# Kernel optimization log

Hardware: AMD Instinct MI355X
Metric: run time of the kernel (lower is better)

The kernel has to match this reference:

```python
import jax, jax.numpy as jnp
import numpy as np

EPS = 1e-5


def _mlp_bn(x, W1, b1, g, beta, W2, b2):
    # Linear -> BatchNorm1d (training: batch stats, biased var) -> ReLU -> Linear
    h = x @ W1 + b1
    mu = h.mean(axis=0)
    var = ((h - mu) ** 2).mean(axis=0)
    h = (h - mu) * jax.lax.rsqrt(var + EPS) * g + beta
    h = jax.nn.relu(h)
    return h @ W2 + b2


def setup_inputs() -> dict:
    key = jax.random.key(0)
    ks = jax.random.split(key, 16)
    B, N, D, K = 32768, 262144, 256, 100
    f32 = jnp.float32
    rn = lambda k, s, sc=1.0: jax.random.normal(k, s, f32) * sc
    inp = {
        "z1": rn(ks[0], (B, D)),
        "z2": rn(ks[1], (B, D)),
        "zn": rn(ks[2], (N, D)),
        "emb": rn(ks[3], (K, D)),
        "proj_W1": rn(ks[4], (D, D), 0.05), "proj_b1": jnp.zeros((D,), f32),
        "proj_g": jnp.ones((D,), f32), "proj_beta": jnp.zeros((D,), f32),
        "proj_W2": rn(ks[5], (D, D), 0.05), "proj_b2": jnp.zeros((D,), f32),
        "invp_W1": rn(ks[6], (D, D), 0.05), "invp_b1": jnp.zeros((D,), f32),
        "invp_g": jnp.ones((D,), f32), "invp_beta": jnp.zeros((D,), f32),
        "invp_W2": rn(ks[7], (D, D), 0.05), "invp_b2": jnp.zeros((D,), f32),
        "latt_W": rn(ks[8], (D, 6), 0.05), "latt_b": jnp.zeros((6,), f32),
        "atom_W": rn(ks[9], (D, K), 0.05), "atom_b": jnp.zeros((K,), f32),
        "scaler_mean": rn(ks[10], (6,)),
        "scaler_std": jax.random.uniform(ks[11], (6,), f32) + 0.5,
        "lscaled_lattice": rn(ks[12], (B, 6)),
        "num_atoms": jnp.full((B,), 8, jnp.int32),
        "batch_idx": (jnp.arange(N) // 8).astype(jnp.int32),
        "atomic_nums": jax.random.randint(ks[13], (N,), 0, K).astype(jnp.int32),
    }
    return inp


def reference(z1, z2, zn, emb,
              proj_W1, proj_b1, proj_g, proj_beta, proj_W2, proj_b2,
              invp_W1, invp_b1, invp_g, invp_beta, invp_W2, invp_b2,
              latt_W, latt_b, atom_W, atom_b,
              scaler_mean, scaler_std, lscaled_lattice,
              num_atoms, batch_idx, atomic_nums):
    sg = jax.lax.stop_gradient
    B = z2.shape[0]
    N = zn.shape[0]

    # ---- VQ: pairwise distances + argmin + gather (get_code_indicies/quantize) ----
    d = (jnp.sum(z2 ** 2, axis=1, keepdims=True)
         + jnp.sum(emb ** 2, axis=1)
         - 2.0 * z2 @ emb.T)                      # [B, K]
    idx = jnp.argmin(d, axis=1)                   # [B]
    quant = emb[idx]                              # [B, D]
    q_latent = jnp.mean((quant - sg(z2)) ** 2)
    e_latent = jnp.mean((z2 - sg(quant)) ** 2)
    vq_loss = q_latent + e_latent
    z2q = z2 + sg(quant - z2)                     # straight-through

    # ---- cycle losses (proj/invp MLPs with train-mode BatchNorm) ----
    p1 = _mlp_bn(z1, proj_W1, proj_b1, proj_g, proj_beta, proj_W2, proj_b2)
    loss_p = jnp.mean((p1 - z2q) ** 2)
    loss_i = jnp.mean((z1 - _mlp_bn(z2q, invp_W1, invp_b1, invp_g, invp_beta, invp_W2, invp_b2)) ** 2)
    loss_c = jnp.mean((_mlp_bn(p1, invp_W1, invp_b1, invp_g, invp_beta, invp_W2, invp_b2) - z1) ** 2)
    cycle_loss = loss_p + loss_i + loss_c

    # ---- lattice loss ----
    pred_la = z2q @ latt_W + latt_b               # [B, 6]
    target_la = (lscaled_lattice - scaler_mean) / scaler_std
    latt_loss = jnp.mean((pred_la - target_la) ** 2) * 10.0

    # ---- per-atom composition cross-entropy, graph-mean then mean ----
    logits = zn @ atom_W + atom_b                 # [N, K]
    logp = jax.nn.log_softmax(logits, axis=-1)
    ce = -jnp.take_along_axis(logp, atomic_nums[:, None].astype(jnp.int32), axis=1)[:, 0]
    sums = jax.ops.segment_sum(ce, batch_idx, num_segments=B)
    counts = jax.ops.segment_sum(jnp.ones_like(ce), batch_idx, num_segments=B)
    atom_loss = jnp.mean(sums / jnp.maximum(counts, 1.0))

    loss = cycle_loss + atom_loss + latt_loss + vq_loss
    return (loss, cycle_loss, atom_loss, latt_loss, vq_loss)
```

## Files before the change

### kernel.cpp

```cpp
#include <hip/hip_runtime.h>
#include <math.h>

#define BATCH 32768
#define DD 256
#define KC 100
#define NATOMS 262144

typedef unsigned short u16;
typedef __attribute__((ext_vector_type(8))) short bf16x8;
typedef __attribute__((ext_vector_type(4))) float f32x4;

union Pack8 { uint4 v; u16 us[8]; };

__device__ inline u16 f2b(float f) {
    unsigned u = __float_as_uint(f);
    unsigned r = (u + 0x7fffu + ((u >> 16) & 1u)) >> 16;
    return (u16)r;
}
__device__ inline float b2f(u16 x) { return __uint_as_float(((unsigned)x) << 16); }


template<int NT>
__device__ inline void block_reduce_add(float v, float* target) {
    __shared__ float red[NT];
    red[threadIdx.x] = v;
    __syncthreads();
    for (int s = NT/2; s > 0; s >>= 1) {
        if ((int)threadIdx.x < s) red[threadIdx.x] += red[threadIdx.x + s];
        __syncthreads();
    }
    if (threadIdx.x == 0) atomicAdd(target, red[0]);
}

__global__ __launch_bounds__(256) void transpose_cvt256_k(const float* __restrict__ W,
                                                          u16* __restrict__ Wt) {
    int o = blockIdx.x * 256 + threadIdx.x;
    int n = o >> 8, k = o & 255;
    Wt[o] = f2b(W[k * 256 + n]);
}
__global__ __launch_bounds__(256) void transpose_cvt_atom_k(const float* __restrict__ W,
                                                            u16* __restrict__ Wt) {
    int o = blockIdx.x * 256 + threadIdx.x;
    int n = o >> 8, k = o & 255;
    Wt[o] = (n < KC) ? f2b(W[k * KC + n]) : (u16)0;
}
__global__ __launch_bounds__(256) void embT_k(const float* __restrict__ emb,
                                              u16* __restrict__ hi, u16* __restrict__ lo) {
    int o = blockIdx.x * 256 + threadIdx.x;
    int n = o >> 8, d = o & 255;
    float v = (n < KC) ? emb[n * DD + d] : 0.f;
    u16 h = f2b(v);
    hi[o] = h;
    lo[o] = f2b(v - b2f(h));
}
__global__ __launch_bounds__(256) void cvt_bf16_k(const float* __restrict__ x,
                                                  u16* __restrict__ y, int n8) {
    int i = blockIdx.x * 256 + threadIdx.x;
    if (i < n8) {
        const float4* p = (const float4*)(x + (size_t)i * 8);
        float4 f0 = p[0], f1 = p[1];
        Pack8 pk;
        pk.us[0]=f2b(f0.x); pk.us[1]=f2b(f0.y); pk.us[2]=f2b(f0.z); pk.us[3]=f2b(f0.w);
        pk.us[4]=f2b(f1.x); pk.us[5]=f2b(f1.y); pk.us[6]=f2b(f1.z); pk.us[7]=f2b(f1.w);
        *(uint4*)(y + (size_t)i * 8) = pk.v;
    }
}
__global__ __launch_bounds__(64) void enorm_k(const float* __restrict__ emb,
                                              float* __restrict__ enorm) {
    int k = blockIdx.x, lane = threadIdx.x;
    float4 v = *(const float4*)(emb + (size_t)k * DD + lane * 4);
    float s = v.x*v.x + v.y*v.y + v.z*v.z + v.w*v.w;
    #pragma unroll
    for (int off = 1; off < 64; off <<= 1) s += __shfl_xor(s, off);
    if (lane == 0) enorm[k] = 0.5f * s;
}

__global__ __launch_bounds__(256) void vq_k(
    const float* __restrict__ z2, const u16* __restrict__ Eh, const u16* __restrict__ El,
    const float* __restrict__ enorm, int* __restrict__ idx, float* acc)
{
    __shared__ u16 Ah[64*32], Al[64*32], Bh[112*32], Bl[112*32];
    const int t = threadIdx.x;
    const int n0 = blockIdx.x * 64;
    const int lane = t & 63, wave = t >> 6;
    const int l15 = lane & 15, lg = lane >> 4;
    const int am = t >> 2, akc = t & 3;

    f32x4 dot[7];
    #pragma unroll
    for (int j = 0; j < 7; ++j) dot[j] = (f32x4){0.f, 0.f, 0.f, 0.f};

    for (int k0 = 0; k0 < DD; k0 += 32) {
        {
            const float* src = z2 + (size_t)(n0 + am) * DD + k0 + akc * 8;
            float4 f0 = *(const float4*)src;
            float4 f1 = *(const float4*)(src + 4);
            float fv[8] = {f0.x, f0.y, f0.z, f0.w, f1.x, f1.y, f1.z, f1.w};
            Pack8 ph, pl;
            #pragma unroll
            for (int e = 0; e < 8; ++e) {
                u16 h = f2b(fv[e]);
                ph.us[e] = h;
                pl.us[e] = f2b(fv[e] - b2f(h));
            }
            int off = (am * 32 + akc * 8) ^ ((am & 7) << 3);
            *(uint4*)(Ah + off) = ph.v;
            *(uint4*)(Al + off) = pl.v;
        }
        {
            int bn = t >> 2, bkc = t & 3;
            int off = (bn * 32 + bkc * 8) ^ ((bn & 7) << 3);
            *(uint4*)(Bh + off) = *(const uint4*)(Eh + bn * DD + k0 + bkc * 8);
            *(uint4*)(Bl + off) = *(const uint4*)(El + bn * DD + k0 + bkc * 8);
            int c2 = t + 256;
            if (c2 < 448) {
                int bn2 = c2 >> 2, bkc2 = c2 & 3;
                int off2 = (bn2 * 32 + bkc2 * 8) ^ ((bn2 & 7) << 3);
                *(uint4*)(Bh + off2) = *(const uint4*)(Eh + bn2 * DD + k0 + bkc2 * 8);
                *(uint4*)(Bl + off2) = *(const uint4*)(El + bn2 * DD + k0 + bkc2 * 8);
            }
        }
        __syncthreads();

        int m = wave * 16 + l15;
        int aoff = (m * 32 + lg * 8) ^ ((m & 7) << 3);
        bf16x8 ah = *(const bf16x8*)(Ah + aoff);
        bf16x8 al = *(const bf16x8*)(Al + aoff);
        #pragma unroll
        for (int j = 0; j < 7; ++j) {
            int n = j * 16 + l15;
            int boff = (n * 32 + lg * 8) ^ ((n & 7) << 3);
            bf16x8 bh = *(const bf16x8*)(Bh + boff);
            bf16x8 bl = *(const bf16x8*)(Bl + boff);
            dot[j] = __builtin_amdgcn_mfma_f32_16x16x32_bf16(ah, bh, dot[j], 0, 0, 0);
            dot[j] = __builtin_amdgcn_mfma_f32_16x16x32_bf16(ah, bl, dot[j], 0, 0, 0);
            dot[j] = __builtin_amdgcn_mfma_f32_16x16x32_bf16(al, bh, dot[j], 0, 0, 0);
        }
        __syncthreads();
    }

    float vq_local = 0.f;
    #pragma unroll
    for (int r = 0; r < 4; ++r) {
        int row = n0 + wave * 16 + lg * 4 + r;
        float bv = 3.4e38f; int bc = 1000;
        #pragma unroll
        for (int j = 0; j < 7; ++j) {
            int c = j * 16 + l15;
            if (c < KC) {
                float y = enorm[c] - dot[j][r];
                if (y < bv) { bv = y; bc = c; }
            }
        }
        #pragma unroll
        for (int off = 1; off < 16; off <<= 1) {
            float ov = __shfl_xor(bv, off);
            int   oc = __shfl_xor(bc, off);
            if (ov < bv || (ov == bv && oc < bc)) { bv = ov; bc = oc; }
        }
        float zs = 0.f;
        const float* zr = z2 + (size_t)row * DD + l15 * 16;
        #pragma unroll
        for (int u = 0; u < 4; ++u) {
            float4 v = *(const float4*)(zr + u * 4);
            zs = fmaf(v.x, v.x, fmaf(v.y, v.y, fmaf(v.z, v.z, fmaf(v.w, v.w, zs))));
        }
        #pragma unroll
        for (int off = 1; off < 16; off <<= 1) zs += __shfl_xor(zs, off);
        if (l15 == 0) {
            idx[row] = bc;
            vq_local += 2.f * bv + zs;
        }
    }
    block_reduce_add<256>(vq_local, acc + 0);
}

template<int MODE_A, int MODE_T, int WRITE_C, int DO_STATS, int DO_LOSS>
__global__ __launch_bounds__(512) void mlp_gemm(
    const void* __restrict__ Asrc, const u16* __restrict__ Wt,
    const float* __restrict__ bias,
    const float* __restrict__ cs_in, const float* __restrict__ cs2_in,
    const float* __restrict__ g_in, const float* __restrict__ beta_in,
    const int* __restrict__ gidx, const float* __restrict__ embf,
    u16* __restrict__ Cb,
    float* __restrict__ colsum, float* __restrict__ colsum2,
    const float* __restrict__ Tf, float* __restrict__ loss_acc)
{
    __shared__ u16 As[64 * 32];
    __shared__ u16 Bs[256 * 32];
    __shared__ float bn_sc[256], bn_sh[256];
    const int t = threadIdx.x;
    const int row0 = blockIdx.x * 64;
    const int lane = t & 63, wave = t >> 6;
    const int wr = wave >> 2, wc = wave & 3;
    const int l15 = lane & 15, lg = lane >> 4;
    const int am = t >> 2, akc = t & 3;

    if (MODE_A == 1) {
        if (t < 256) {
            float mu  = cs_in[t]  * (1.f / (float)BATCH);
            float var = cs2_in[t] * (1.f / (float)BATCH) - mu * mu;
            float sc = g_in[t] * rsqrtf(var + 1e-5f);
            bn_sc[t] = sc;
            bn_sh[t] = beta_in[t] - mu * sc;
        }
        __syncthreads();
    }

    f32x4 acc[2][4];
    #pragma unroll
    for (int mt = 0; mt < 2; ++mt)
        #pragma unroll
        for (int j = 0; j < 4; ++j)
            acc[mt][j] = (f32x4){0.f, 0.f, 0.f, 0.f};

    for (int k0 = 0; k0 < DD; k0 += 32) {
        if (t < 256) {
            uint4 d;
            if (MODE_A == 3) {
                const float* src = (const float*)Asrc + (size_t)(row0 + am) * DD + k0 + akc * 8;
                float4 f0 = *(const float4*)src;
                float4 f1 = *(const float4*)(src + 4);
                Pack8 pk;
                pk.us[0]=f2b(f0.x); pk.us[1]=f2b(f0.y); pk.us[2]=f2b(f0.z); pk.us[3]=f2b(f0.w);
                pk.us[4]=f2b(f1.x); pk.us[5]=f2b(f1.y); pk.us[6]=f2b(f1.z); pk.us[7]=f2b(f1.w);
                d = pk.v;
            } else if (MODE_A == 2) {
                int code = gidx[row0 + am];
                d = *(const uint4*)((const u16*)Asrc + (size_t)code * DD + k0 + akc * 8);
            } else {
                d = *(const uint4*)((const u16*)Asrc + (size_t)(row0 + am) * DD + k0 + akc * 8);
            }
            if (MODE_A == 1) {
                Pack8 pk; pk.v = d;
                #pragma unroll
                for (int e = 0; e < 8; ++e) {
                    int k = k0 + akc * 8 + e;
                    float v = fmaf(b2f(pk.us[e]), bn_sc[k], bn_sh[k]);
                    pk.us[e] = f2b(v > 0.f ? v : 0.f);
                }
                d = pk.v;
            }
            *(uint4*)(As + ((am * 32 + akc * 8) ^ ((am & 7) << 3))) = d;
        }
        #pragma unroll
        for (int q = 0; q < 2; ++q) {
            int ch = t * 2 + q;
            int bn = ch >> 2, bkc = ch & 3;
            uint4 d = *(const uint4*)(Wt + bn * DD + k0 + bkc * 8);
            *(uint4*)(Bs + ((bn * 32 + bkc * 8) ^ ((bn & 7) << 3))) = d;
        }
        __syncthreads();

        bf16x8 af[2], bfr[4];
        #pragma unroll
        for (int mt = 0; mt < 2; ++mt) {
            int m = wr * 32 + mt * 16 + l15;
            af[mt] = *(const bf16x8*)(As + ((m * 32 + lg * 8) ^ ((m & 7) << 3)));
        }
        #pragma unroll
        for (int j = 0; j < 4; ++j) {
            int n = wc * 64 + j * 16 + l15;
            bfr[j] = *(const bf16x8*)(Bs + ((n * 32 + lg * 8) ^ ((n & 7) << 3)));
        }
        #pragma unroll
        for (int mt = 0; mt < 2; ++mt)
            #pragma unroll
            for (int j = 0; j < 4; ++j)
                acc[mt][j] = __builtin_amdgcn_mfma_f32_16x16x32_bf16(af[mt], bfr[j], acc[mt][j], 0, 0, 0);
        __syncthreads();
    }

    float lsum = 0.f;
    #pragma unroll
    for (int j = 0; j < 4; ++j) {
        int c = wc * 64 + j * 16 + l15;
        float bc = bias[c];
        float cs = 0.f, cs2 = 0.f;
        #pragma unroll
        for (int mt = 0; mt < 2; ++mt) {
            #pragma unroll
            for (int r = 0; r < 4; ++r) {
                int row = row0 + wr * 32 + mt * 16 + lg * 4 + r;
                float y = acc[mt][j][r] + bc;
                if (WRITE_C) Cb[(size_t)row * DD + c] = f2b(y);
                if (DO_STATS) { cs += y; cs2 = fmaf(y, y, cs2); }
                if (DO_LOSS) {
                    float tv = (MODE_T == 2) ? embf[(size_t)gidx[row] * DD + c]
                                             : Tf[(size_t)row * DD + c];
                    float dd = y - tv;
                    lsum = fmaf(dd, dd, lsum);
                }
            }
        }
        if (DO_STATS) {
            cs  += __shfl_xor(cs, 16);  cs  += __shfl_xor(cs, 32);
            cs2 += __shfl_xor(cs2, 16); cs2 += __shfl_xor(cs2, 32);
            if (lg == 0) {
                atomicAdd(&colsum[c], cs);
                atomicAdd(&colsum2[c], cs2);
            }
        }
    }
    if (DO_LOSS) block_reduce_add<512>(lsum, loss_acc);
}

__global__ __launch_bounds__(256) void latt_k(
    const float* __restrict__ emb, const int* __restrict__ idx,
    const float* __restrict__ lattW, const float* __restrict__ lattb,
    const float* __restrict__ smean, const float* __restrict__ sstd,
    const float* __restrict__ lsc, float* acc)
{
    __shared__ float lwT[6][256];
    const int t = threadIdx.x, lane = t & 63, wave = t >> 6;
    for (int o = t; o < 1536; o += 256) {
        int d = o / 6, j = o - d * 6;
        lwT[j][d] = lattW[o];
    }
    __syncthreads();
    float s = 0.f;
    const int b0 = blockIdx.x * 32 + wave * 8;
    for (int rr = 0; rr < 8; ++rr) {
        int b = b0 + rr;
        const float* q = emb + (size_t)idx[b] * DD;
        float a[6] = {0.f,0.f,0.f,0.f,0.f,0.f};
        #pragma unroll
        for (int dd = 0; dd < 4; ++dd) {
            int d = lane + dd * 64;
            float qv = q[d];
            #pragma unroll
            for (int j = 0; j < 6; ++j) a[j] = fmaf(qv, lwT[j][d], a[j]);
        }
        #pragma unroll
        for (int j = 0; j < 6; ++j) {
            #pragma unroll
            for (int off = 1; off < 64; off <<= 1) a[j] += __shfl_xor(a[j], off);
        }
        if (lane == 0) {
            #pragma unroll
            for (int j = 0; j < 6; ++j) {
                float pred = a[j] + lattb[j];
                float tgt = (lsc[(size_t)b * 6 + j] - smean[j]) / sstd[j];
                float dd2 = pred - tgt;
                s = fmaf(dd2, dd2, s);
            }
        }
    }
    block_reduce_add<256>(s, acc + 4);
}

__global__ __launch_bounds__(256) void atom_k(
    const float* __restrict__ zn, const u16* __restrict__ Wat, const float* __restrict__ ba,
    const int* __restrict__ atomic_nums, const int* __restrict__ batch_idx,
    float* __restrict__ gsums, float* __restrict__ gcnts)
{
    __shared__ u16 As[64 * 32];
    __shared__ u16 Bs[112 * 32];
    const int t = threadIdx.x;
    const int n0 = blockIdx.x * 64;
    const int lane = t & 63, wave = t >> 6;
    const int l15 = lane & 15, lg = lane >> 4;
    const int am = t >> 2, akc = t & 3;

    f32x4 acc[7];
    #pragma unroll
    for (int j = 0; j < 7; ++j) acc[j] = (f32x4){0.f, 0.f, 0.f, 0.f};

    for (int k0 = 0; k0 < DD; k0 += 32) {
        {
            const float* src = zn + (size_t)(n0 + am) * DD + k0 + akc * 8;
            float4 f0 = *(const float4*)src;
            float4 f1 = *(const float4*)(src + 4);
            Pack8 pk;
            pk.us[0]=f2b(f0.x); pk.us[1]=f2b(f0.y); pk.us[2]=f2b(f0.z); pk.us[3]=f2b(f0.w);
            pk.us[4]=f2b(f1.x); pk.us[5]=f2b(f1.y); pk.us[6]=f2b(f1.z); pk.us[7]=f2b(f1.w);
            *(uint4*)(As + ((am * 32 + akc * 8) ^ ((am & 7) << 3))) = pk.v;
        }
        {
            int bn = t >> 2, bkc = t & 3;
            uint4 d = *(const uint4*)(Wat + bn * DD + k0 + bkc * 8);
            *(uint4*)(Bs + ((bn * 32 + bkc * 8) ^ ((bn & 7) << 3))) = d;
            int ch = t + 256;
            if (ch < 448) {
                int bn2 = ch >> 2, bkc2 = ch & 3;
                uint4 d2 = *(const uint4*)(Wat + bn2 * DD + k0 + bkc2 * 8);
                *(uint4*)(Bs + ((bn2 * 32 + bkc2 * 8) ^ ((bn2 & 7) << 3))) = d2;
            }
        }
        __syncthreads();

        int m = wave * 16 + l15;
        bf16x8 af = *(const bf16x8*)(As + ((m * 32 + lg * 8) ^ ((m & 7) << 3)));
        #pragma unroll
        for (int j = 0; j < 7; ++j) {
            int n = j * 16 + l15;
            bf16x8 bfv = *(const bf16x8*)(Bs + ((n * 32 + lg * 8) ^ ((n & 7) << 3)));
            acc[j] = __builtin_amdgcn_mfma_f32_16x16x32_bf16(af, bfv, acc[j], 0, 0, 0);
        }
        __syncthreads();
    }

    #pragma unroll
    for (int r = 0; r < 4; ++r) {
        float y[7];
        float mx = -3.4e38f;
        #pragma unroll
        for (int j = 0; j < 7; ++j) {
            int c = j * 16 + l15;
            y[j] = (c < KC) ? (acc[j][r] + ba[c]) : -3.4e38f;
            mx = fmaxf(mx, y[j]);
        }
        mx = fmaxf(mx, __shfl_xor(mx, 1));
        mx = fmaxf(mx, __shfl_xor(mx, 2));
        mx = fmaxf(mx, __shfl_xor(mx, 4));
        mx = fmaxf(mx, __shfl_xor(mx, 8));
        float s = 0.f;
        #pragma unroll
        for (int j = 0; j < 7; ++j) {
            int c = j * 16 + l15;
            if (c < KC) s += expf(y[j] - mx);
        }
        s += __shfl_xor(s, 1); s += __shfl_xor(s, 2);
        s += __shfl_xor(s, 4); s += __shfl_xor(s, 8);
        int n = n0 + wave * 16 + lg * 4 + r;
        int tgt = atomic_nums[n];
        float tv = 0.f;
        #pragma unroll
        for (int j = 0; j < 7; ++j)
            tv += (((tgt & 15) == l15) && ((tgt >> 4) == j)) ? y[j] : 0.f;
        tv += __shfl_xor(tv, 1); tv += __shfl_xor(tv, 2);
        tv += __shfl_xor(tv, 4); tv += __shfl_xor(tv, 8);
        if (l15 == 0) {
            float ce = logf(s) + mx - tv;
            int b = batch_idx[n];
            atomicAdd(&gsums[b], ce);
            atomicAdd(&gcnts[b], 1.f);
        }
    }
}

__global__ __launch_bounds__(256) void atom_final_k(const float* __restrict__ gsums,
                                                    const float* __restrict__ gcnts,
                                                    float* acc) {
    int b = blockIdx.x * 256 + threadIdx.x;
    float v = gsums[b] / fmaxf(gcnts[b], 1.f);
    block_reduce_add<256>(v, acc + 5);
}

__global__ void finalize_k(const float* __restrict__ acc, float* __restrict__ out) {
    if (threadIdx.x == 0) {
        const float inv_bd = 1.f / ((float)BATCH * (float)DD);
        float cyc = (acc[1] + acc[2] + acc[3]) * inv_bd;
        float vq = 2.f * acc[0] * inv_bd;
        float latt = acc[4] / ((float)BATCH * 6.f) * 10.f;
        float atom = acc[5] * (1.f / (float)BATCH);
        out[0] = cyc + atom + latt + vq;
        out[1] = cyc;
        out[2] = atom;
        out[3] = latt;
        out[4] = vq;
    }
}

extern "C" void kernel_launch(void* const* d_in, const int* in_sizes, int n_in,
                              void* d_out, int out_size, void* d_ws, size_t ws_size,
                              hipStream_t stream)
{
    const float* z1      = (const float*)d_in[0];
    const float* z2      = (const float*)d_in[1];
    const float* zn      = (const float*)d_in[2];
    const float* emb     = (const float*)d_in[3];
    const float* proj_W1 = (const float*)d_in[4];
    const float* proj_b1 = (const float*)d_in[5];
    const float* proj_g  = (const float*)d_in[6];
    const float* proj_be = (const float*)d_in[7];
    const float* proj_W2 = (const float*)d_in[8];
    const float* proj_b2 = (const float*)d_in[9];
    const float* invp_W1 = (const float*)d_in[10];
    const float* invp_b1 = (const float*)d_in[11];
    const float* invp_g  = (const float*)d_in[12];
    const float* invp_be = (const float*)d_in[13];
    const float* invp_W2 = (const float*)d_in[14];
    const float* invp_b2 = (const float*)d_in[15];
    const float* latt_W  = (const float*)d_in[16];
    const float* latt_b  = (const float*)d_in[17];
    const float* atom_W  = (const float*)d_in[18];
    const float* atom_b  = (const float*)d_in[19];
    const float* smean   = (const float*)d_in[20];
    const float* sstd    = (const float*)d_in[21];
    const float* lsc     = (const float*)d_in[22];
    const int* batch_idx   = (const int*)d_in[24];
    const int* atomic_nums = (const int*)d_in[25];
    float* out = (float*)d_out;
    float* ws  = (float*)d_ws;

    float* acc     = ws + 0;
    float* colsum  = ws + 16;
    float* colsum2 = ws + 784;
    float* gsums   = ws + 1552;
    float* gcnts   = ws + 34320;
    float* enorm   = ws + 67088;
    int*   idx     = (int*)(ws + 67216);
    u16* wt_proj1  = (u16*)(ws + 100000);
    u16* wt_proj2  = (u16*)(ws + 132768);
    u16* wt_invp1  = (u16*)(ws + 165536);
    u16* wt_invp2  = (u16*)(ws + 198304);
    u16* wat       = (u16*)(ws + 231072);
    u16* embT_hi   = (u16*)(ws + 245408);
    u16* embT_lo   = (u16*)(ws + 259744);
    u16* emb_b     = (u16*)(ws + 274080);
    u16* h_b       = (u16*)(ws + 286880);
    u16* p1_b      = (u16*)(ws + 4481184);

    hipMemsetAsync(d_ws, 0, 67088 * sizeof(float), stream);

    transpose_cvt256_k<<<256, 256, 0, stream>>>(proj_W1, wt_proj1);
    transpose_cvt256_k<<<256, 256, 0, stream>>>(proj_W2, wt_proj2);
    transpose_cvt256_k<<<256, 256, 0, stream>>>(invp_W1, wt_invp1);
    transpose_cvt256_k<<<256, 256, 0, stream>>>(invp_W2, wt_invp2);
    transpose_cvt_atom_k<<<112, 256, 0, stream>>>(atom_W, wat);
    embT_k<<<112, 256, 0, stream>>>(emb, embT_hi, embT_lo);
    cvt_bf16_k<<<13, 256, 0, stream>>>(emb, emb_b, KC * DD / 8);
    enorm_k<<<KC, 64, 0, stream>>>(emb, enorm);

    vq_k<<<512, 256, 0, stream>>>(z2, embT_hi, embT_lo, enorm, idx, acc);

    mlp_gemm<3,1,1,1,0><<<512, 512, 0, stream>>>(z1, wt_proj1, proj_b1,
        nullptr, nullptr, nullptr, nullptr, idx, emb, h_b, colsum+0, colsum2+0, nullptr, nullptr);
    mlp_gemm<1,2,1,0,1><<<512, 512, 0, stream>>>(h_b, wt_proj2, proj_b2,
        colsum+0, colsum2+0, proj_g, proj_be, idx, emb, p1_b, nullptr, nullptr, nullptr, acc+1);
    mlp_gemm<2,1,1,1,0><<<512, 512, 0, stream>>>(emb_b, wt_invp1, invp_b1,
        nullptr, nullptr, nullptr, nullptr, idx, emb, h_b, colsum+256, colsum2+256, nullptr, nullptr);
    mlp_gemm<1,1,0,0,1><<<512, 512, 0, stream>>>(h_b, wt_invp2, invp_b2,
        colsum+256, colsum2+256, invp_g, invp_be, idx, emb, nullptr, nullptr, nullptr, z1, acc+2);
    mlp_gemm<0,1,1,1,0><<<512, 512, 0, stream>>>(p1_b, wt_invp1, invp_b1,
        nullptr, nullptr, nullptr, nullptr, idx, emb, h_b, colsum+512, colsum2+512, nullptr, nullptr);
    mlp_gemm<1,1,0,0,1><<<512, 512, 0, stream>>>(h_b, wt_invp2, invp_b2,
        colsum+512, colsum2+512, invp_g, invp_be, idx, emb, nullptr, nullptr, nullptr, z1, acc+3);

    latt_k<<<1024, 256, 0, stream>>>(emb, idx, latt_W, latt_b, smean, sstd, lsc, acc);
    atom_k<<<4096, 256, 0, stream>>>(zn, wat, atom_b, atomic_nums, batch_idx, gsums, gcnts);
    atom_final_k<<<128, 256, 0, stream>>>(gsums, gcnts, acc);
    finalize_k<<<1, 64, 0, stream>>>(acc, out);
}
```

Measured before the change: 731.6 us.

## Fuse setup kernels, use hardware bf16 pack, reuse z2 norms, retile MLP GEMM

Merges the eight small weight-conversion, embedding-split and norm kernels into a single setup launch to cut launch overhead. Replaces software float-to-bf16 rounding with the packed v_cvt_pk_bf16_f32 instruction in all staging paths. The VQ kernel now accumulates row squared norms while staging z2 instead of re-reading z2 in the epilogue. The MLP GEMM tiles change from 64x256 to 128x128 per block, splitting columns across two blocks so A and B staging is balanced over all 512 threads, at the cost of re-reading each A row twice.

```diff
diff --git a/kernel.cpp b/kernel.cpp
--- a/kernel.cpp
+++ b/kernel.cpp
@@ -18,6 +18,17 @@
     return (u16)r;
 }
 __device__ inline float b2f(u16 x) { return __uint_as_float(((unsigned)x) << 16); }
+__device__ inline unsigned cvtpk(float lo, float hi) {
+    unsigned r;
+    asm("v_cvt_pk_bf16_f32 %0, %1, %2" : "=v"(r) : "v"(lo), "v"(hi));
+    return r;
+}
+__device__ inline uint4 pack8(float4 a, float4 b) {
+    uint4 r;
+    r.x = cvtpk(a.x, a.y); r.y = cvtpk(a.z, a.w);
+    r.z = cvtpk(b.x, b.y); r.w = cvtpk(b.z, b.w);
+    return r;
+}
 
 
 template<int NT>
@@ -32,47 +43,51 @@
     if (threadIdx.x == 0) atomicAdd(target, red[0]);
 }
 
-__global__ __launch_bounds__(256) void transpose_cvt256_k(const float* __restrict__ W,
-                                                          u16* __restrict__ Wt) {
-    int o = blockIdx.x * 256 + threadIdx.x;
-    int n = o >> 8, k = o & 255;
-    Wt[o] = f2b(W[k * 256 + n]);
-}
-__global__ __launch_bounds__(256) void transpose_cvt_atom_k(const float* __restrict__ W,
-                                                            u16* __restrict__ Wt) {
-    int o = blockIdx.x * 256 + threadIdx.x;
-    int n = o >> 8, k = o & 255;
-    Wt[o] = (n < KC) ? f2b(W[k * KC + n]) : (u16)0;
-}
-__global__ __launch_bounds__(256) void embT_k(const float* __restrict__ emb,
-                                              u16* __restrict__ hi, u16* __restrict__ lo) {
-    int o = blockIdx.x * 256 + threadIdx.x;
-    int n = o >> 8, d = o & 255;
-    float v = (n < KC) ? emb[n * DD + d] : 0.f;
-    u16 h = f2b(v);
-    hi[o] = h;
-    lo[o] = f2b(v - b2f(h));
-}
-__global__ __launch_bounds__(256) void cvt_bf16_k(const float* __restrict__ x,
-                                                  u16* __restrict__ y, int n8) {
-    int i = blockIdx.x * 256 + threadIdx.x;
-    if (i < n8) {
-        const float4* p = (const float4*)(x + (size_t)i * 8);
-        float4 f0 = p[0], f1 = p[1];
-        Pack8 pk;
-        pk.us[0]=f2b(f0.x); pk.us[1]=f2b(f0.y); pk.us[2]=f2b(f0.z); pk.us[3]=f2b(f0.w);
-        pk.us[4]=f2b(f1.x); pk.us[5]=f2b(f1.y); pk.us[6]=f2b(f1.z); pk.us[7]=f2b(f1.w);
-        *(uint4*)(y + (size_t)i * 8) = pk.v;
-    }
-}
-__global__ __launch_bounds__(64) void enorm_k(const float* __restrict__ emb,
-                                              float* __restrict__ enorm) {
-    int k = blockIdx.x, lane = threadIdx.x;
-    float4 v = *(const float4*)(emb + (size_t)k * DD + lane * 4);
-    float s = v.x*v.x + v.y*v.y + v.z*v.z + v.w*v.w;
-    #pragma unroll
-    for (int off = 1; off < 64; off <<= 1) s += __shfl_xor(s, off);
-    if (lane == 0) enorm[k] = 0.5f * s;
+__global__ __launch_bounds__(256) void setup_k(
+    const float* __restrict__ pW1, const float* __restrict__ pW2,
+    const float* __restrict__ iW1, const float* __restrict__ iW2,
+    const float* __restrict__ aW, const float* __restrict__ emb,
+    u16* __restrict__ wtp1, u16* __restrict__ wtp2,
+    u16* __restrict__ wti1, u16* __restrict__ wti2,
+    u16* __restrict__ wat, u16* __restrict__ eh, u16* __restrict__ el,
+    u16* __restrict__ embb, float* __restrict__ enorm)
+{
+    const int blk = blockIdx.x, t = threadIdx.x;
+    if (blk < 1024) {
+        int g = blk >> 8;
+        const float* W = (g == 0) ? pW1 : (g == 1) ? pW2 : (g == 2) ? iW1 : iW2;
+        u16* Wt = (g == 0) ? wtp1 : (g == 1) ? wtp2 : (g == 2) ? wti1 : wti2;
+        int o = (blk & 255) * 256 + t;
+        int n = o >> 8, k = o & 255;
+        Wt[o] = f2b(W[k * 256 + n]);
+    } else if (blk < 1136) {
+        int o = (blk - 1024) * 256 + t;
+        int n = o >> 8, k = o & 255;
+        wat[o] = (n < KC) ? f2b(aW[k * KC + n]) : (u16)0;
+    } else if (blk < 1248) {
+        int o = (blk - 1136) * 256 + t;
+        int n = o >> 8, d = o & 255;
+        float v = (n < KC) ? emb[n * DD + d] : 0.f;
+        u16 h = f2b(v);
+        eh[o] = h;
+        el[o] = f2b(v - b2f(h));
+    } else if (blk < 1255) {
+        int i = (blk - 1248) * 256 + t;
+        if (i < 1600) {
+            const float4* p = (const float4*)(emb + (size_t)i * 8);
+            *(uint4*)(embb + (size_t)i * 8) = pack8(p[0], p[1]);
+        }
+    } else {
+        int row = (blk - 1255) * 4 + (t >> 6);
+        int lane = t & 63;
+        if (row < KC) {
+            float4 v = *(const float4*)(emb + (size_t)row * DD + lane * 4);
+            float s = v.x*v.x + v.y*v.y + v.z*v.z + v.w*v.w;
+            #pragma unroll
+            for (int off = 1; off < 64; off <<= 1) s += __shfl_xor(s, off);
+            if (lane == 0) enorm[row] = 0.5f * s;
+        }
+    }
 }
 
 __global__ __launch_bounds__(256) void vq_k(
@@ -80,6 +95,7 @@
     const float* __restrict__ enorm, int* __restrict__ idx, float* acc)
 {
     __shared__ u16 Ah[64*32], Al[64*32], Bh[112*32], Bl[112*32];
+    __shared__ float zrow[64];
     const int t = threadIdx.x;
     const int n0 = blockIdx.x * 64;
     const int lane = t & 63, wave = t >> 6;
@@ -89,23 +105,24 @@
     f32x4 dot[7];
     #pragma unroll
     for (int j = 0; j < 7; ++j) dot[j] = (f32x4){0.f, 0.f, 0.f, 0.f};
+    float zsq = 0.f;
 
     for (int k0 = 0; k0 < DD; k0 += 32) {
         {
             const float* src = z2 + (size_t)(n0 + am) * DD + k0 + akc * 8;
             float4 f0 = *(const float4*)src;
             float4 f1 = *(const float4*)(src + 4);
-            float fv[8] = {f0.x, f0.y, f0.z, f0.w, f1.x, f1.y, f1.z, f1.w};
-            Pack8 ph, pl;
-            #pragma unroll
-            for (int e = 0; e < 8; ++e) {
-                u16 h = f2b(fv[e]);
-                ph.us[e] = h;
-                pl.us[e] = f2b(fv[e] - b2f(h));
-            }
+            zsq += f0.x*f0.x + f0.y*f0.y + f0.z*f0.z + f0.w*f0.w
+                 + f1.x*f1.x + f1.y*f1.y + f1.z*f1.z + f1.w*f1.w;
+            uint4 hv = pack8(f0, f1);
+            Pack8 ph; ph.v = hv;
+            float4 l0 = make_float4(f0.x - b2f(ph.us[0]), f0.y - b2f(ph.us[1]),
+                                    f0.z - b2f(ph.us[2]), f0.w - b2f(ph.us[3]));
+            float4 l1 = make_float4(f1.x - b2f(ph.us[4]), f1.y - b2f(ph.us[5]),
+                                    f1.z - b2f(ph.us[6]), f1.w - b2f(ph.us[7]));
             int off = (am * 32 + akc * 8) ^ ((am & 7) << 3);
-            *(uint4*)(Ah + off) = ph.v;
-            *(uint4*)(Al + off) = pl.v;
+            *(uint4*)(Ah + off) = hv;
+            *(uint4*)(Al + off) = pack8(l0, l1);
         }
         {
             int bn = t >> 2, bkc = t & 3;
@@ -139,6 +156,11 @@
         __syncthreads();
     }
 
+    zsq += __shfl_xor(zsq, 1);
+    zsq += __shfl_xor(zsq, 2);
+    if ((t & 3) == 0) zrow[am] = zsq;
+    __syncthreads();
+
     float vq_local = 0.f;
     #pragma unroll
     for (int r = 0; r < 4; ++r) {
@@ -158,18 +180,9 @@
             int   oc = __shfl_xor(bc, off);
             if (ov < bv || (ov == bv && oc < bc)) { bv = ov; bc = oc; }
         }
-        float zs = 0.f;
-        const float* zr = z2 + (size_t)row * DD + l15 * 16;
-        #pragma unroll
-        for (int u = 0; u < 4; ++u) {
-            float4 v = *(const float4*)(zr + u * 4);
-            zs = fmaf(v.x, v.x, fmaf(v.y, v.y, fmaf(v.z, v.z, fmaf(v.w, v.w, zs))));
-        }
-        #pragma unroll
-        for (int off = 1; off < 16; off <<= 1) zs += __shfl_xor(zs, off);
         if (l15 == 0) {
             idx[row] = bc;
-            vq_local += 2.f * bv + zs;
+            vq_local += 2.f * bv + zrow[row - n0];
         }
     }
     block_reduce_add<256>(vq_local, acc + 0);
@@ -186,15 +199,17 @@
     float* __restrict__ colsum, float* __restrict__ colsum2,
     const float* __restrict__ Tf, float* __restrict__ loss_acc)
 {
-    __shared__ u16 As[64 * 32];
-    __shared__ u16 Bs[256 * 32];
+    __shared__ u16 As[128 * 32];
+    __shared__ u16 Bs[128 * 32];
     __shared__ float bn_sc[256], bn_sh[256];
     const int t = threadIdx.x;
-    const int row0 = blockIdx.x * 64;
+    const int bid = blockIdx.x;
+    const int row0 = (bid >> 1) * 128;
+    const int col0 = (bid & 1) * 128;
     const int lane = t & 63, wave = t >> 6;
-    const int wr = wave >> 2, wc = wave & 3;
+    const int wm = wave >> 1, wn = wave & 1;
     const int l15 = lane & 15, lg = lane >> 4;
-    const int am = t >> 2, akc = t & 3;
+    const int sr = t >> 2, skc = t & 3;
 
     if (MODE_A == 1) {
         if (t < 256) {
@@ -215,52 +230,46 @@
             acc[mt][j] = (f32x4){0.f, 0.f, 0.f, 0.f};
 
     for (int k0 = 0; k0 < DD; k0 += 32) {
-        if (t < 256) {
+        {
             uint4 d;
             if (MODE_A == 3) {
-                const float* src = (const float*)Asrc + (size_t)(row0 + am) * DD + k0 + akc * 8;
-                float4 f0 = *(const float4*)src;
-                float4 f1 = *(const float4*)(src + 4);
-                Pack8 pk;
-                pk.us[0]=f2b(f0.x); pk.us[1]=f2b(f0.y); pk.us[2]=f2b(f0.z); pk.us[3]=f2b(f0.w);
-                pk.us[4]=f2b(f1.x); pk.us[5]=f2b(f1.y); pk.us[6]=f2b(f1.z); pk.us[7]=f2b(f1.w);
-                d = pk.v;
+                const float* src = (const float*)Asrc + (size_t)(row0 + sr) * DD + k0 + skc * 8;
+                d = pack8(*(const float4*)src, *(const float4*)(src + 4));
             } else if (MODE_A == 2) {
-                int code = gidx[row0 + am];
-                d = *(const uint4*)((const u16*)Asrc + (size_t)code * DD + k0 + akc * 8);
+                int code = gidx[row0 + sr];
+                d = *(const uint4*)((const u16*)Asrc + (size_t)code * DD + k0 + skc * 8);
             } else {
-                d = *(const uint4*)((const u16*)Asrc + (size_t)(row0 + am) * DD + k0 + akc * 8);
+                d = *(const uint4*)((const u16*)Asrc + (size_t)(row0 + sr) * DD + k0 + skc * 8);
             }
             if (MODE_A == 1) {
                 Pack8 pk; pk.v = d;
+                float f[8];
                 #pragma unroll
                 for (int e = 0; e < 8; ++e) {
-                    int k = k0 + akc * 8 + e;
+                    int k = k0 + skc * 8 + e;
                     float v = fmaf(b2f(pk.us[e]), bn_sc[k], bn_sh[k]);
-                    pk.us[e] = f2b(v > 0.f ? v : 0.f);
+                    f[e] = v > 0.f ? v : 0.f;
                 }
-                d = pk.v;
-            }
-            *(uint4*)(As + ((am * 32 + akc * 8) ^ ((am & 7) << 3))) = d;
-        }
-        #pragma unroll
-        for (int q = 0; q < 2; ++q) {
-            int ch = t * 2 + q;
-            int bn = ch >> 2, bkc = ch & 3;
-            uint4 d = *(const uint4*)(Wt + bn * DD + k0 + bkc * 8);
-            *(uint4*)(Bs + ((bn * 32 + bkc * 8) ^ ((bn & 7) << 3))) = d;
+                d = pack8(make_float4(f[0], f[1], f[2], f[3]),
+                          make_float4(f[4], f[5], f[6], f[7]));
+            }
+            *(uint4*)(As + ((sr * 32 + skc * 8) ^ ((sr & 7) << 3))) = d;
+        }
+        {
+            uint4 d = *(const uint4*)(Wt + (size_t)(col0 + sr) * DD + k0 + skc * 8);
+            *(uint4*)(Bs + ((sr * 32 + skc * 8) ^ ((sr & 7) << 3))) = d;
         }
         __syncthreads();
 
         bf16x8 af[2], bfr[4];
         #pragma unroll
         for (int mt = 0; mt < 2; ++mt) {
-            int m = wr * 32 + mt * 16 + l15;
+            int m = wm * 32 + mt * 16 + l15;
             af[mt] = *(const bf16x8*)(As + ((m * 32 + lg * 8) ^ ((m & 7) << 3)));
         }
         #pragma unroll
         for (int j = 0; j < 4; ++j) {
-            int n = wc * 64 + j * 16 + l15;
+            int n = wn * 64 + j * 16 + l15;
             bfr[j] = *(const bf16x8*)(Bs + ((n * 32 + lg * 8) ^ ((n & 7) << 3)));
         }
         #pragma unroll
@@ -274,14 +283,14 @@
     float lsum = 0.f;
     #pragma unroll
     for (int j = 0; j < 4; ++j) {
-        int c = wc * 64 + j * 16 + l15;
+        int c = col0 + wn * 64 + j * 16 + l15;
         float bc = bias[c];
         float cs = 0.f, cs2 = 0.f;
         #pragma unroll
         for (int mt = 0; mt < 2; ++mt) {
             #pragma unroll
             for (int r = 0; r < 4; ++r) {
-                int row = row0 + wr * 32 + mt * 16 + lg * 4 + r;
+                int row = row0 + wm * 32 + mt * 16 + lg * 4 + r;
                 float y = acc[mt][j][r] + bc;
                 if (WRITE_C) Cb[(size_t)row * DD + c] = f2b(y);
                 if (DO_STATS) { cs += y; cs2 = fmaf(y, y, cs2); }
@@ -369,12 +378,8 @@
     for (int k0 = 0; k0 < DD; k0 += 32) {
         {
             const float* src = zn + (size_t)(n0 + am) * DD + k0 + akc * 8;
-            float4 f0 = *(const float4*)src;
-            float4 f1 = *(const float4*)(src + 4);
-            Pack8 pk;
-            pk.us[0]=f2b(f0.x); pk.us[1]=f2b(f0.y); pk.us[2]=f2b(f0.z); pk.us[3]=f2b(f0.w);
-            pk.us[4]=f2b(f1.x); pk.us[5]=f2b(f1.y); pk.us[6]=f2b(f1.z); pk.us[7]=f2b(f1.w);
-            *(uint4*)(As + ((am * 32 + akc * 8) ^ ((am & 7) << 3))) = pk.v;
+            uint4 d = pack8(*(const float4*)src, *(const float4*)(src + 4));
+            *(uint4*)(As + ((am * 32 + akc * 8) ^ ((am & 7) << 3))) = d;
         }
         {
             int bn = t >> 2, bkc = t & 3;
@@ -514,14 +519,8 @@
 
     hipMemsetAsync(d_ws, 0, 67088 * sizeof(float), stream);
 
-    transpose_cvt256_k<<<256, 256, 0, stream>>>(proj_W1, wt_proj1);
-    transpose_cvt256_k<<<256, 256, 0, stream>>>(proj_W2, wt_proj2);
-    transpose_cvt256_k<<<256, 256, 0, stream>>>(invp_W1, wt_invp1);
-    transpose_cvt256_k<<<256, 256, 0, stream>>>(invp_W2, wt_invp2);
-    transpose_cvt_atom_k<<<112, 256, 0, stream>>>(atom_W, wat);
-    embT_k<<<112, 256, 0, stream>>>(emb, embT_hi, embT_lo);
-    cvt_bf16_k<<<13, 256, 0, stream>>>(emb, emb_b, KC * DD / 8);
-    enorm_k<<<KC, 64, 0, stream>>>(emb, enorm);
+    setup_k<<<1280, 256, 0, stream>>>(proj_W1, proj_W2, invp_W1, invp_W2, atom_W, emb,
+        wt_proj1, wt_proj2, wt_invp1, wt_invp2, wat, embT_hi, embT_lo, emb_b, enorm);
 
     vq_k<<<512, 256, 0, stream>>>(z2, embT_hi, embT_lo, enorm, idx, acc);
 
```

Measured after the change: 718.8 us. Within noise of the previous version (-1.7%).
